# Performance work log

Hardware: AMD Instinct MI355X
Metric: run time of the kernel (lower is better)

## Reference

```python
import jax, jax.numpy as jnp
import numpy as np

GRID_SIZE = 8
MARGIN = 1.0
NUM_NEG = 8
SOS_NEG = 8
LOSS_LAMBDA = 1.0
D_INTER = 4  # d1_inter_num == d2_inter_num == 4 in the source
IMG = 512    # image side in pixels (H * grid_size)


def warp_points(pts, homo):
    ph = jnp.concatenate([pts, jnp.ones_like(pts[..., :1])], axis=-1)  # B,N,3
    q = jnp.einsum('bij,bnj->bni', homo, ph)
    return q[..., :2] / (q[..., 2:3] + 1e-8)


def inv_sim_vec(d1, d2):
    # 2 - 2*<d1,d2> == squared L2 distance for unit-norm descriptors
    return 2.0 - 2.0 * jnp.sum(d1 * d2, axis=-1)


def inv_sim_mat(d1, d2):
    return 2.0 - 2.0 * jnp.einsum('bnc,bmc->bnm', d1, d2)


def sq_dist_mat(p1, p2):
    # squared Euclidean distance; monotone in distance so topk indices and
    # radius comparisons (vs radius**2) match the original exactly.
    n1 = jnp.sum(p1 * p1, axis=-1)
    n2 = jnp.sum(p2 * p2, axis=-1)
    d = n1[:, :, None] + n2[:, None, :] - 2.0 * jnp.einsum('bnd,bmd->bnm', p1, p2)
    return jnp.maximum(d, 0.0)


def topk_smallest(x, k):
    v, i = jax.lax.top_k(-x, k)
    return -v, i


def create_coo_grid(h, w, grid_size):
    ys, xs = jnp.meshgrid(jnp.arange(h, dtype=jnp.float32), jnp.arange(w, dtype=jnp.float32), indexing='ij')
    return jnp.stack([(xs + 0.5) * grid_size, (ys + 0.5) * grid_size], axis=-1).reshape(-1, 2)  # HW,2 (x,y)


def sample_descriptors(desc, kp, grid_size):
    # desc: B,C,H,W; kp: B,N,2 (x,y) image coords. Bilinear sample + L2 normalize.
    b, c, h, w = desc.shape
    x = kp[..., 0] / grid_size - 0.5
    y = kp[..., 1] / grid_size - 0.5
    x0 = jnp.floor(x); y0 = jnp.floor(y)
    wx = x - x0; wy = y - y0
    x0i = jnp.clip(x0.astype(jnp.int32), 0, w - 1); x1i = jnp.clip(x0i + 1, 0, w - 1)
    y0i = jnp.clip(y0.astype(jnp.int32), 0, h - 1); y1i = jnp.clip(y0i + 1, 0, h - 1)
    dflat = desc.transpose(0, 2, 3, 1).reshape(b, h * w, c)  # B,HW,C
    bi = jnp.arange(b)[:, None]
    g = lambda yi, xi: dflat[bi, yi * w + xi]  # B,N,C
    out = ((1 - wx) * (1 - wy))[..., None] * g(y0i, x0i) \
        + (wx * (1 - wy))[..., None] * g(y0i, x1i) \
        + ((1 - wx) * wy)[..., None] * g(y1i, x0i) \
        + (wx * wy)[..., None] * g(y1i, x1i)
    return out / (jnp.linalg.norm(out, axis=-1, keepdims=True) + 1e-8)


def setup_inputs():
    key = jax.random.key(0)
    k1, k2, k3, k4 = jax.random.split(key, 4)
    b, n, c, h, w = 4, 1024, 128, 64, 64
    kp1 = jax.random.uniform(k1, (b, n, 2), dtype=jnp.float32) * (IMG - 1.0)
    kp1_desc = jax.random.normal(k2, (b, n, c), dtype=jnp.float32)
    kp1_desc = kp1_desc / jnp.linalg.norm(kp1_desc, axis=-1, keepdims=True)
    desc2 = jax.random.normal(k3, (b, c, h, w), dtype=jnp.float32)
    homo12 = jnp.broadcast_to(jnp.eye(3, dtype=jnp.float32), (b, 3, 3)) + 0.005 * jax.random.normal(k4, (b, 3, 3), dtype=jnp.float32)
    w_kp1 = jnp.clip(warp_points(kp1, homo12), 0.0, IMG - 1.0)
    return {'kp1': kp1, 'w_kp1': w_kp1, 'kp1_desc': kp1_desc, 'desc2': desc2, 'homo12': homo12}


def reference(kp1, w_kp1, kp1_desc, desc2, homo12):
    b, n, c = kp1_desc.shape
    _, _, h, w = desc2.shape
    hw = h * w
    gs = GRID_SIZE
    bi = jnp.arange(b)[:, None]

    w_kp1_desc = sample_descriptors(desc2, w_kp1, gs)                 # B,N,C
    positive_sim = inv_sim_vec(kp1_desc, w_kp1_desc)                  # B,N

    coo = jnp.broadcast_to(create_coo_grid(h, w, gs), (b, hw, 2))     # B,HW,2
    # 4 nearest grid cells of each kp1, warped into image 2
    _, kp1_cell_ids = topk_smallest(sq_dist_mat(kp1, coo), D_INTER)   # B,N,4
    kp1_cells = coo[bi, kp1_cell_ids.reshape(b, -1)]                  # B,4N,2
    w_kp1_cells = warp_points(kp1_cells, homo12)                      # B,4N,2
    _, kp2_cell_ids = topk_smallest(sq_dist_mat(w_kp1_cells, coo), D_INTER)  # B,4N,4
    mask = jnp.zeros((b, n * D_INTER, hw), dtype=jnp.float32)
    mask = mask.at[jnp.arange(b)[:, None, None], jnp.arange(n * D_INTER)[None, :, None], kp2_cell_ids].set(1.0)
    neigh_mask = mask.reshape(b, n, D_INTER, hw).sum(axis=2)          # B,N,HW

    desc2_flat = desc2.transpose(0, 2, 3, 1).reshape(b, hw, c)
    desc_sim = inv_sim_mat(kp1_desc, desc2_flat) + neigh_mask * 5.0   # B,N,HW
    neg_sim, _ = topk_smallest(desc_sim, NUM_NEG)                     # B,N,num_neg
    fos = jnp.mean(jnp.maximum(positive_sim[:, :, None] - neg_sim + MARGIN, 0.0) ** 2)

    radius2 = (gs * np.sqrt(2.0) + 0.1) ** 2
    kp1_sim = inv_sim_mat(kp1_desc, kp1_desc) + (sq_dist_mat(kp1, kp1) <= radius2).astype(jnp.float32) * 5.0
    w_kp1_sim = inv_sim_mat(w_kp1_desc, w_kp1_desc) + (sq_dist_mat(w_kp1, w_kp1) <= radius2).astype(jnp.float32) * 5.0
    _, kp1_neg_ids = topk_smallest(kp1_sim, SOS_NEG)                  # B,N,sos_neg
    _, w_kp1_neg_ids = topk_smallest(w_kp1_sim, SOS_NEG)
    b3 = jnp.arange(b)[:, None, None]
    kp1_neg_desc = kp1_desc[b3, kp1_neg_ids]                          # B,N,sos_neg,C
    w_kp1_neg_desc = w_kp1_desc[b3, w_kp1_neg_ids]
    sos = inv_sim_vec(kp1_desc[:, :, None, :], kp1_neg_desc) - inv_sim_vec(w_kp1_desc[:, :, None, :], w_kp1_neg_desc)
    sos = jnp.mean(jnp.sqrt(jnp.sum(sos ** 2, axis=-1)))
    return (fos + sos) * LOSS_LAMBDA
```

## Files before the change

kernel.cpp:

```cpp
#include <hip/hip_runtime.h>

#define NB 4
#define NN 1024
#define NCCH 128
#define NH 64
#define NW 64
#define NHW 4096

constexpr float RADIUS2 = 130.27274173013714f;

typedef __attribute__((ext_vector_type(8))) short short8v;
typedef __attribute__((ext_vector_type(4))) float f32x4;

__device__ __forceinline__ unsigned short f2bf(float f) {
    unsigned u = __float_as_uint(f);
    unsigned r = u + 0x7FFFu + ((u >> 16) & 1u);
    return (unsigned short)(r >> 16);
}
__device__ __forceinline__ float bf2f(unsigned short h) {
    return __uint_as_float(((unsigned)h) << 16);
}

__device__ __forceinline__ void bsort8(float* v) {
    #pragma unroll
    for (int d = 4; d >= 1; d >>= 1) {
        #pragma unroll
        for (int i = 0; i < 8; ++i) {
            if ((i & d) == 0) {
                float x = v[i], y = v[i + d];
                v[i] = fminf(x, y);
                v[i + d] = fmaxf(x, y);
            }
        }
    }
}
__device__ __forceinline__ void merge8(const float* a, const float* b, float* o) {
    #pragma unroll
    for (int k = 0; k < 8; ++k) o[k] = fminf(a[k], b[7 - k]);
    bsort8(o);
}

__device__ __forceinline__ void nearest4(float x, float y, int out_ids[4]) {
    float u = x * 0.125f - 0.5f;
    float v = y * 0.125f - 0.5f;
    u = fminf(fmaxf(u, -1e6f), 1e6f);
    v = fminf(fmaxf(v, -1e6f), 1e6f);
    int iu = (int)floorf(u);
    int iv = (int)floorf(v);
    int xlo = min(max(iu - 2, 0), 60);
    int xhi = max(min(iu + 3, 63), 3);
    int ylo = min(max(iv - 2, 0), 60);
    int yhi = max(min(iv + 3, 63), 3);
    float bd0 = 1e30f, bd1 = 1e30f, bd2 = 1e30f, bd3 = 1e30f;
    int bi0 = 0, bi1 = 0, bi2 = 0, bi3 = 0;
    for (int yy = ylo; yy <= yhi; ++yy) {
        float dy = y - ((float)yy + 0.5f) * 8.0f;
        float dy2 = dy * dy;
        for (int xx = xlo; xx <= xhi; ++xx) {
            float dx = x - ((float)xx + 0.5f) * 8.0f;
            float d = dx * dx + dy2;
            int id = (yy << 6) | xx;
            if (d < bd3) {
                if (d < bd2) {
                    bd3 = bd2; bi3 = bi2;
                    if (d < bd1) {
                        bd2 = bd1; bi2 = bi1;
                        if (d < bd0) { bd1 = bd0; bi1 = bi0; bd0 = d; bi0 = id; }
                        else         { bd1 = d;  bi1 = id; }
                    } else { bd2 = d; bi2 = id; }
                } else { bd3 = d; bi3 = id; }
            }
        }
    }
    out_ids[0] = bi0; out_ids[1] = bi1; out_ids[2] = bi2; out_ids[3] = bi3;
}

__global__ __launch_bounds__(256) void sample_kernel(
    const float* __restrict__ kp1, const float* __restrict__ w_kp1,
    const float* __restrict__ kp1_desc, const float* __restrict__ desc2,
    unsigned short* __restrict__ khi, unsigned short* __restrict__ klo,
    unsigned short* __restrict__ whi, unsigned short* __restrict__ wlo,
    float* __restrict__ pos_sim)
{
    int lane = threadIdx.x & 63;
    int wid = blockIdx.x * 4 + (threadIdx.x >> 6);
    if (wid >= NB * NN) return;
    int b = wid >> 10;

    float px = w_kp1[wid * 2 + 0], py = w_kp1[wid * 2 + 1];
    float fx = px * 0.125f - 0.5f, fy = py * 0.125f - 0.5f;
    float fx0 = floorf(fx), fy0 = floorf(fy);
    float wx = fx - fx0, wy = fy - fy0;
    int x0 = min(max((int)fx0, 0), NW - 1);
    int x1 = min(x0 + 1, NW - 1);
    int y0 = min(max((int)fy0, 0), NH - 1);
    int y1 = min(y0 + 1, NH - 1);
    float w00 = (1.f - wx) * (1.f - wy), w01 = wx * (1.f - wy);
    float w10 = (1.f - wx) * wy,         w11 = wx * wy;
    int i00 = y0 * NW + x0, i01 = y0 * NW + x1;
    int i10 = y1 * NW + x0, i11 = y1 * NW + x1;

    const float* d2 = desc2 + (size_t)b * NCCH * NHW;
    const float* p0 = d2 + (size_t)lane * NHW;
    const float* p1 = d2 + (size_t)(lane + 64) * NHW;
    float o0 = w00 * p0[i00] + w01 * p0[i01] + w10 * p0[i10] + w11 * p0[i11];
    float o1 = w00 * p1[i00] + w01 * p1[i01] + w10 * p1[i10] + w11 * p1[i11];
    float nrm = o0 * o0 + o1 * o1;
    #pragma unroll
    for (int off = 32; off > 0; off >>= 1) nrm += __shfl_xor(nrm, off, 64);
    float inv = 1.0f / (sqrtf(nrm) + 1e-8f);
    o0 *= inv; o1 *= inv;

    float a0 = kp1_desc[(size_t)wid * NCCH + lane];
    float a1 = kp1_desc[(size_t)wid * NCCH + lane + 64];
    float dot = a0 * o0 + a1 * o1;
    #pragma unroll
    for (int off = 32; off > 0; off >>= 1) dot += __shfl_xor(dot, off, 64);

    size_t base = (size_t)wid * NCCH;
    unsigned short h;
    h = f2bf(a0); khi[base + lane] = h;      klo[base + lane] = f2bf(a0 - bf2f(h));
    h = f2bf(a1); khi[base + lane + 64] = h; klo[base + lane + 64] = f2bf(a1 - bf2f(h));
    h = f2bf(o0); whi[base + lane] = h;      wlo[base + lane] = f2bf(o0 - bf2f(h));
    h = f2bf(o1); whi[base + lane + 64] = h; wlo[base + lane + 64] = f2bf(o1 - bf2f(h));
    if (lane == 0) pos_sim[wid] = 2.0f - 2.0f * dot;
}

__global__ __launch_bounds__(256) void d2split_kernel(
    const float* __restrict__ desc2,
    unsigned short* __restrict__ d2hi, unsigned short* __restrict__ d2lo)
{
    __shared__ float sT[64][130];
    int b = blockIdx.x >> 6;
    int hw0 = (blockIdx.x & 63) * 64;
    int t = threadIdx.x;
    int hwl = t & 63, cg = t >> 6;
    const float* src = desc2 + (size_t)b * NCCH * NHW + hw0 + hwl;
    #pragma unroll 4
    for (int i = 0; i < 32; ++i) {
        int c = cg * 32 + i;
        sT[hwl][c] = src[(size_t)c * NHW];
    }
    __syncthreads();
    int hw = t >> 2, cseg = (t & 3) * 32;
    unsigned short* dh = d2hi + ((size_t)b * NHW + hw0 + hw) * NCCH + cseg;
    unsigned short* dl = d2lo + ((size_t)b * NHW + hw0 + hw) * NCCH + cseg;
    #pragma unroll 4
    for (int i = 0; i < 32; ++i) {
        float f = sT[hw][cseg + i];
        unsigned short h = f2bf(f);
        dh[i] = h;
        dl[i] = f2bf(f - bf2f(h));
    }
}

__global__ __launch_bounds__(256) void mask_kernel(
    const float* __restrict__ kp1, const float* __restrict__ homo,
    int* __restrict__ mask_ids)
{
    int g = blockIdx.x * blockDim.x + threadIdx.x;
    if (g >= NB * NN) return;
    int b = g >> 10;
    float x = kp1[g * 2], y = kp1[g * 2 + 1];
    const float* H = homo + b * 9;
    int c4[4];
    nearest4(x, y, c4);
    int out[16];
    #pragma unroll
    for (int k = 0; k < 4; ++k) {
        int id = c4[k];
        float cx = ((float)(id & 63) + 0.5f) * 8.0f;
        float cy = ((float)(id >> 6) + 0.5f) * 8.0f;
        float q0 = H[0] * cx + H[1] * cy + H[2];
        float q1 = H[3] * cx + H[4] * cy + H[5];
        float q2 = H[6] * cx + H[7] * cy + H[8];
        float iz = 1.0f / (q2 + 1e-8f);
        nearest4(q0 * iz, q1 * iz, out + 4 * k);
    }
    #pragma unroll
    for (int k = 0; k < 16; ++k) mask_ids[(size_t)g * 16 + k] = out[k];
}

__global__ __launch_bounds__(256, 4) void simtop_fused(
    const unsigned short* __restrict__ khi, const unsigned short* __restrict__ klo,
    const unsigned short* __restrict__ whi, const unsigned short* __restrict__ wlo,
    const unsigned short* __restrict__ d2hi, const unsigned short* __restrict__ d2lo,
    const float* __restrict__ kp1, const float* __restrict__ w_kp1,
    const int* __restrict__ mask_ids,
    float* __restrict__ fosP, float* __restrict__ sosAP, float* __restrict__ sosBP)
{
    __shared__ float sChunk[16][257];
    __shared__ int   sMask[16][16];
    __shared__ float sCx[256], sCy[256];
    __shared__ float sRx[16], sRy[16];

    int tid = threadIdx.x;
    int bid = blockIdx.x;

    int mode, cs, rg, b, nchunk, colbase, outStride;
    const unsigned short *AH, *AL, *BH, *BL;
    const float* coords = nullptr;
    float* outP;
    if (bid < 1024) {
        mode = 0; cs = bid & 3; rg = (bid >> 2) & 63; b = bid >> 8;
        nchunk = 4; colbase = cs * 1024;
        AH = khi + (size_t)b * NN * NCCH;  AL = klo + (size_t)b * NN * NCCH;
        BH = d2hi + (size_t)b * NHW * NCCH; BL = d2lo + (size_t)b * NHW * NCCH;
        outP = fosP; outStride = 32;
    } else if (bid < 1536) {
        int id = bid - 1024;
        mode = 1; cs = id & 1; rg = (id >> 1) & 63; b = id >> 7;
        nchunk = 2; colbase = cs * 512;
        AH = khi + (size_t)b * NN * NCCH;  AL = klo + (size_t)b * NN * NCCH;
        BH = AH; BL = AL;
        coords = kp1; outP = sosAP; outStride = 16;
    } else {
        int id = bid - 1536;
        mode = 2; cs = id & 1; rg = (id >> 1) & 63; b = id >> 7;
        nchunk = 2; colbase = cs * 512;
        AH = whi + (size_t)b * NN * NCCH;  AL = wlo + (size_t)b * NN * NCCH;
        BH = AH; BL = AL;
        coords = w_kp1; outP = sosBP; outStride = 16;
    }
    int row0 = rg * 16;

    int lane = tid & 63, wg = tid >> 6;
    int lrow = lane & 15, lgrp = lane >> 4;
    int srow = tid & 15, sgrp = tid >> 4;

    short8v ahi[4], alo[4];
    {
        const unsigned short* aH = AH + (size_t)(row0 + lrow) * NCCH + lgrp * 8;
        const unsigned short* aL = AL + (size_t)(row0 + lrow) * NCCH + lgrp * 8;
        #pragma unroll
        for (int s = 0; s < 4; ++s) {
            ahi[s] = *(const short8v*)(aH + s * 32);
            alo[s] = *(const short8v*)(aL + s * 32);
        }
    }

    if (mode == 0) {
        sMask[tid >> 4][tid & 15] =
            mask_ids[((size_t)b * NN + row0 + (tid >> 4)) * 16 + (tid & 15)];
    } else if (tid < 16) {
        sRx[tid] = coords[((size_t)b * NN + row0 + tid) * 2];
        sRy[tid] = coords[((size_t)b * NN + row0 + tid) * 2 + 1];
    }

    float loc[8];
    #pragma unroll
    for (int k = 0; k < 8; ++k) loc[k] = 1e30f;

    for (int ch = 0; ch < nchunk; ++ch) {
        int cglob = colbase + ch * 256;
        __syncthreads();

        int colq = cglob + wg * 64;
        #pragma unroll
        for (int nt = 0; nt < 4; ++nt) {
            const unsigned short* bH = BH + (size_t)(colq + nt * 16 + lrow) * NCCH + lgrp * 8;
            const unsigned short* bL = BL + (size_t)(colq + nt * 16 + lrow) * NCCH + lgrp * 8;
            f32x4 acc = {0.f, 0.f, 0.f, 0.f};
            #pragma unroll
            for (int s = 0; s < 4; ++s) {
                short8v bhv = *(const short8v*)(bH + s * 32);
                short8v blv = *(const short8v*)(bL + s * 32);
                acc = __builtin_amdgcn_mfma_f32_16x16x32_bf16(ahi[s], bhv, acc, 0, 0, 0);
                acc = __builtin_amdgcn_mfma_f32_16x16x32_bf16(ahi[s], blv, acc, 0, 0, 0);
                acc = __builtin_amdgcn_mfma_f32_16x16x32_bf16(alo[s], bhv, acc, 0, 0, 0);
            }
            #pragma unroll
            for (int r = 0; r < 4; ++r)
                sChunk[lgrp * 4 + r][wg * 64 + nt * 16 + lrow] = 2.0f - 2.0f * acc[r];
        }
        __syncthreads();

        if (mode == 0) {
            int r = tid >> 4, k = tid & 15;
            int id = sMask[r][k] - cglob;
            if (id >= 0 && id < 256) atomicAdd(&sChunk[r][id], 5.0f);
        } else {
            sCx[tid] = coords[((size_t)b * NN + cglob + tid) * 2];
            sCy[tid] = coords[((size_t)b * NN + cglob + tid) * 2 + 1];
        }
        __syncthreads();

        float rx = 0.f, ry = 0.f;
        if (mode != 0) { rx = sRx[srow]; ry = sRy[srow]; }
        #pragma unroll
        for (int j = 0; j < 16; ++j) {
            int cl = sgrp * 16 + j;
            float v = sChunk[srow][cl];
            if (mode != 0) {
                float dx = rx - sCx[cl], dy = ry - sCy[cl];
                if (dx * dx + dy * dy <= RADIUS2) v += 5.0f;
            }
            if (v < loc[7]) {
                loc[7] = v;
                #pragma unroll
                for (int p = 7; p > 0; --p) {
                    if (loc[p - 1] > loc[p]) {
                        float t = loc[p - 1]; loc[p - 1] = loc[p]; loc[p] = t;
                    }
                }
            }
        }
    }

    __syncthreads();
    float* mg = &sChunk[0][0];
    #pragma unroll
    for (int k = 0; k < 8; ++k) mg[srow * 130 + sgrp * 8 + k] = loc[k];
    __syncthreads();
    #pragma unroll
    for (int step = 1; step < 16; step <<= 1) {
        if ((sgrp & (2 * step - 1)) == 0) {
            float a[8], bb[8], o[8];
            #pragma unroll
            for (int k = 0; k < 8; ++k) {
                a[k]  = mg[srow * 130 + sgrp * 8 + k];
                bb[k] = mg[srow * 130 + (sgrp + step) * 8 + k];
            }
            merge8(a, bb, o);
            #pragma unroll
            for (int k = 0; k < 8; ++k) mg[srow * 130 + sgrp * 8 + k] = o[k];
        }
        __syncthreads();
    }
    if (tid < 16) {
        size_t row = (size_t)b * NN + row0 + tid;
        #pragma unroll
        for (int k = 0; k < 8; ++k)
            outP[row * outStride + cs * 8 + k] = mg[tid * 130 + k];
    }
}

__global__ __launch_bounds__(256) void frow_kernel(
    const float* __restrict__ fosP, const float* __restrict__ sosAP,
    const float* __restrict__ sosBP, const float* __restrict__ pos_sim,
    float* __restrict__ frow, float* __restrict__ srow)
{
    int row = blockIdx.x * 256 + threadIdx.x;
    if (row >= NB * NN) return;

    float l0[8], l1[8], l2[8], l3[8], t0[8], t1[8], m[8];
    const float4* fp = (const float4*)(fosP + (size_t)row * 32);
    float4 q;
    q = fp[0]; l0[0]=q.x; l0[1]=q.y; l0[2]=q.z; l0[3]=q.w;
    q = fp[1]; l0[4]=q.x; l0[5]=q.y; l0[6]=q.z; l0[7]=q.w;
    q = fp[2]; l1[0]=q.x; l1[1]=q.y; l1[2]=q.z; l1[3]=q.w;
    q = fp[3]; l1[4]=q.x; l1[5]=q.y; l1[6]=q.z; l1[7]=q.w;
    q = fp[4]; l2[0]=q.x; l2[1]=q.y; l2[2]=q.z; l2[3]=q.w;
    q = fp[5]; l2[4]=q.x; l2[5]=q.y; l2[6]=q.z; l2[7]=q.w;
    q = fp[6]; l3[0]=q.x; l3[1]=q.y; l3[2]=q.z; l3[3]=q.w;
    q = fp[7]; l3[4]=q.x; l3[5]=q.y; l3[6]=q.z; l3[7]=q.w;
    merge8(l0, l1, t0); merge8(l2, l3, t1); merge8(t0, t1, m);

    float p = pos_sim[row], fs = 0.f;
    #pragma unroll
    for (int k = 0; k < 8; ++k) {
        float h = fmaxf(p - m[k] + 1.0f, 0.f);
        fs += h * h;
    }

    const float4* ap = (const float4*)(sosAP + (size_t)row * 16);
    q = ap[0]; l0[0]=q.x; l0[1]=q.y; l0[2]=q.z; l0[3]=q.w;
    q = ap[1]; l0[4]=q.x; l0[5]=q.y; l0[6]=q.z; l0[7]=q.w;
    q = ap[2]; l1[0]=q.x; l1[1]=q.y; l1[2]=q.z; l1[3]=q.w;
    q = ap[3]; l1[4]=q.x; l1[5]=q.y; l1[6]=q.z; l1[7]=q.w;
    merge8(l0, l1, t0);
    const float4* bp = (const float4*)(sosBP + (size_t)row * 16);
    q = bp[0]; l2[0]=q.x; l2[1]=q.y; l2[2]=q.z; l2[3]=q.w;
    q = bp[1]; l2[4]=q.x; l2[5]=q.y; l2[6]=q.z; l2[7]=q.w;
    q = bp[2]; l3[0]=q.x; l3[1]=q.y; l3[2]=q.z; l3[3]=q.w;
    q = bp[3]; l3[4]=q.x; l3[5]=q.y; l3[6]=q.z; l3[7]=q.w;
    merge8(l2, l3, t1);

    float acc = 0.f;
    #pragma unroll
    for (int k = 0; k < 8; ++k) {
        float d = t0[k] - t1[k];
        acc += d * d;
    }
    frow[row] = fs;
    srow[row] = sqrtf(acc);
}

__global__ __launch_bounds__(256) void freduce_kernel(
    const float* __restrict__ frow, const float* __restrict__ srow,
    float* __restrict__ outp)
{
    __shared__ float sf[256], ss[256];
    int t = threadIdx.x;
    float f = 0.f, s = 0.f;
    for (int i = t; i < NB * NN; i += 256) { f += frow[i]; s += srow[i]; }
    sf[t] = f; ss[t] = s;
    __syncthreads();
    for (int o = 128; o > 0; o >>= 1) {
        if (t < o) { sf[t] += sf[t + o]; ss[t] += ss[t + o]; }
        __syncthreads();
    }
    if (t == 0)
        outp[0] = sf[0] / (float)(NB * NN * 8) + ss[0] / (float)(NB * NN);
}

extern "C" void kernel_launch(void* const* d_in, const int* in_sizes, int n_in,
                              void* d_out, int out_size, void* d_ws, size_t ws_size,
                              hipStream_t stream) {
    const float* kp1      = (const float*)d_in[0];
    const float* w_kp1    = (const float*)d_in[1];
    const float* kp1_desc = (const float*)d_in[2];
    const float* desc2    = (const float*)d_in[3];
    const float* homo     = (const float*)d_in[4];
    float* outp = (float*)d_out;

    char* ws = (char*)d_ws;
    size_t o = 0;
    unsigned short* khi  = (unsigned short*)(ws + o); o += (size_t)NB * NN * NCCH * 2;
    unsigned short* klo  = (unsigned short*)(ws + o); o += (size_t)NB * NN * NCCH * 2;
    unsigned short* whi  = (unsigned short*)(ws + o); o += (size_t)NB * NN * NCCH * 2;
    unsigned short* wlo  = (unsigned short*)(ws + o); o += (size_t)NB * NN * NCCH * 2;
    unsigned short* d2hi = (unsigned short*)(ws + o); o += (size_t)NB * NHW * NCCH * 2;
    unsigned short* d2lo = (unsigned short*)(ws + o); o += (size_t)NB * NHW * NCCH * 2;
    float* pos_sim = (float*)(ws + o); o += (size_t)NB * NN * 4;
    float* fosP    = (float*)(ws + o); o += (size_t)NB * NN * 32 * 4;
    float* sosAP   = (float*)(ws + o); o += (size_t)NB * NN * 16 * 4;
    float* sosBP   = (float*)(ws + o); o += (size_t)NB * NN * 16 * 4;
    float* frow    = (float*)(ws + o); o += (size_t)NB * NN * 4;
    float* srow    = (float*)(ws + o); o += (size_t)NB * NN * 4;
    int*   mask_id = (int*)(ws + o);   o += (size_t)NB * NN * 16 * 4;

    sample_kernel<<<NB * NN / 4, 256, 0, stream>>>(kp1, w_kp1, kp1_desc, desc2,
                                                   khi, klo, whi, wlo, pos_sim);
    d2split_kernel<<<NB * 64, 256, 0, stream>>>(desc2, d2hi, d2lo);
    mask_kernel<<<NB * NN / 256, 256, 0, stream>>>(kp1, homo, mask_id);
    simtop_fused<<<2048, 256, 0, stream>>>(khi, klo, whi, wlo, d2hi, d2lo,
                                           kp1, w_kp1, mask_id,
                                           fosP, sosAP, sosBP);
    frow_kernel<<<16, 256, 0, stream>>>(fosP, sosAP, sosBP, pos_sim, frow, srow);
    freduce_kernel<<<1, 256, 0, stream>>>(frow, srow, outp);
}
```

Measured before the change: 211.8 us.

## Widen simtop row tiles to 32, fuse sample+mask, transpose desc2 for sampling

The similarity/top-k kernel now processes 32 rows per block using a 2x2 MFMA register tile, so each loaded B fragment is reused across two row tiles. This halves the grid and the B-operand global traffic. The d2split kernel is re-tiled with vectorized stores and optionally writes an fp32 HWC transpose of desc2, which the sampling path reads with coalesced row accesses instead of strided channel gathers. Sampling and mask computation are merged into one launch. The changes raise register and shared memory pressure in the top-k kernel and add an extra fp32 write of desc2, which may be skipped if the workspace is too small.

```diff
diff --git a/kernel.cpp b/kernel.cpp
--- a/kernel.cpp
+++ b/kernel.cpp
@@ -75,16 +75,88 @@
     out_ids[0] = bi0; out_ids[1] = bi1; out_ids[2] = bi2; out_ids[3] = bi3;
 }
 
-__global__ __launch_bounds__(256) void sample_kernel(
+__global__ __launch_bounds__(256) void d2split_kernel(
+    const float* __restrict__ desc2,
+    unsigned short* __restrict__ d2hi, unsigned short* __restrict__ d2lo,
+    float* __restrict__ d2T, int use_t)
+{
+    __shared__ float sT[64][33];
+    int bid = blockIdx.x;
+    int b = bid >> 8;
+    int rem = bid & 255;
+    int hw0 = (rem >> 2) * 64;
+    int c0 = (rem & 3) * 32;
+    int t = threadIdx.x;
+
+    {
+        int lane = t & 63, cg = t >> 6;
+        const float* src = desc2 + (size_t)b * NCCH * NHW + hw0 + lane;
+        #pragma unroll
+        for (int i = 0; i < 8; ++i) {
+            int cl = cg * 8 + i;
+            sT[lane][cl] = src[(size_t)(c0 + cl) * NHW];
+        }
+    }
+    __syncthreads();
+    {
+        int hw = t >> 2, q = t & 3;
+        size_t base = ((size_t)b * NHW + hw0 + hw) * NCCH + c0 + q * 8;
+        unsigned short hb[8], lb[8];
+        float fb[8];
+        #pragma unroll
+        for (int i = 0; i < 8; ++i) {
+            float f = sT[hw][q * 8 + i];
+            unsigned short h = f2bf(f);
+            hb[i] = h;
+            lb[i] = f2bf(f - bf2f(h));
+            fb[i] = f;
+        }
+        *(short8v*)(d2hi + base) = *(short8v*)hb;
+        *(short8v*)(d2lo + base) = *(short8v*)lb;
+        if (use_t) {
+            *(float4*)(d2T + base) = *(float4*)&fb[0];
+            *(float4*)(d2T + base + 4) = *(float4*)&fb[4];
+        }
+    }
+}
+
+__global__ __launch_bounds__(256) void sample_mask_kernel(
     const float* __restrict__ kp1, const float* __restrict__ w_kp1,
     const float* __restrict__ kp1_desc, const float* __restrict__ desc2,
+    const float* __restrict__ d2T, int use_t,
+    const float* __restrict__ homo,
     unsigned short* __restrict__ khi, unsigned short* __restrict__ klo,
     unsigned short* __restrict__ whi, unsigned short* __restrict__ wlo,
-    float* __restrict__ pos_sim)
+    float* __restrict__ pos_sim, int* __restrict__ mask_ids)
 {
+    int bid = blockIdx.x;
+    if (bid >= 1024) {
+        int g = (bid - 1024) * 256 + threadIdx.x;
+        if (g >= NB * NN) return;
+        int b = g >> 10;
+        float x = kp1[g * 2], y = kp1[g * 2 + 1];
+        const float* H = homo + b * 9;
+        int c4[4];
+        nearest4(x, y, c4);
+        int out[16];
+        #pragma unroll
+        for (int k = 0; k < 4; ++k) {
+            int id = c4[k];
+            float cx = ((float)(id & 63) + 0.5f) * 8.0f;
+            float cy = ((float)(id >> 6) + 0.5f) * 8.0f;
+            float q0 = H[0] * cx + H[1] * cy + H[2];
+            float q1 = H[3] * cx + H[4] * cy + H[5];
+            float q2 = H[6] * cx + H[7] * cy + H[8];
+            float iz = 1.0f / (q2 + 1e-8f);
+            nearest4(q0 * iz, q1 * iz, out + 4 * k);
+        }
+        #pragma unroll
+        for (int k = 0; k < 16; ++k) mask_ids[(size_t)g * 16 + k] = out[k];
+        return;
+    }
+
     int lane = threadIdx.x & 63;
-    int wid = blockIdx.x * 4 + (threadIdx.x >> 6);
-    if (wid >= NB * NN) return;
+    int wid = bid * 4 + (threadIdx.x >> 6);
     int b = wid >> 10;
 
     float px = w_kp1[wid * 2 + 0], py = w_kp1[wid * 2 + 1];
@@ -100,11 +172,23 @@
     int i00 = y0 * NW + x0, i01 = y0 * NW + x1;
     int i10 = y1 * NW + x0, i11 = y1 * NW + x1;
 
-    const float* d2 = desc2 + (size_t)b * NCCH * NHW;
-    const float* p0 = d2 + (size_t)lane * NHW;
-    const float* p1 = d2 + (size_t)(lane + 64) * NHW;
-    float o0 = w00 * p0[i00] + w01 * p0[i01] + w10 * p0[i10] + w11 * p0[i11];
-    float o1 = w00 * p1[i00] + w01 * p1[i01] + w10 * p1[i10] + w11 * p1[i11];
+    float o0, o1;
+    if (use_t) {
+        const float* base = d2T + (size_t)b * NHW * NCCH;
+        const float* r00 = base + (size_t)i00 * NCCH;
+        const float* r01 = base + (size_t)i01 * NCCH;
+        const float* r10 = base + (size_t)i10 * NCCH;
+        const float* r11 = base + (size_t)i11 * NCCH;
+        o0 = w00 * r00[lane] + w01 * r01[lane] + w10 * r10[lane] + w11 * r11[lane];
+        o1 = w00 * r00[lane + 64] + w01 * r01[lane + 64]
+           + w10 * r10[lane + 64] + w11 * r11[lane + 64];
+    } else {
+        const float* d2 = desc2 + (size_t)b * NCCH * NHW;
+        const float* p0 = d2 + (size_t)lane * NHW;
+        const float* p1 = d2 + (size_t)(lane + 64) * NHW;
+        o0 = w00 * p0[i00] + w01 * p0[i01] + w10 * p0[i10] + w11 * p0[i11];
+        o1 = w00 * p1[i00] + w01 * p1[i01] + w10 * p1[i10] + w11 * p1[i11];
+    }
     float nrm = o0 * o0 + o1 * o1;
     #pragma unroll
     for (int off = 32; off > 0; off >>= 1) nrm += __shfl_xor(nrm, off, 64);
@@ -124,61 +208,6 @@
     h = f2bf(o0); whi[base + lane] = h;      wlo[base + lane] = f2bf(o0 - bf2f(h));
     h = f2bf(o1); whi[base + lane + 64] = h; wlo[base + lane + 64] = f2bf(o1 - bf2f(h));
     if (lane == 0) pos_sim[wid] = 2.0f - 2.0f * dot;
-}
-
-__global__ __launch_bounds__(256) void d2split_kernel(
-    const float* __restrict__ desc2,
-    unsigned short* __restrict__ d2hi, unsigned short* __restrict__ d2lo)
-{
-    __shared__ float sT[64][130];
-    int b = blockIdx.x >> 6;
-    int hw0 = (blockIdx.x & 63) * 64;
-    int t = threadIdx.x;
-    int hwl = t & 63, cg = t >> 6;
-    const float* src = desc2 + (size_t)b * NCCH * NHW + hw0 + hwl;
-    #pragma unroll 4
-    for (int i = 0; i < 32; ++i) {
-        int c = cg * 32 + i;
-        sT[hwl][c] = src[(size_t)c * NHW];
-    }
-    __syncthreads();
-    int hw = t >> 2, cseg = (t & 3) * 32;
-    unsigned short* dh = d2hi + ((size_t)b * NHW + hw0 + hw) * NCCH + cseg;
-    unsigned short* dl = d2lo + ((size_t)b * NHW + hw0 + hw) * NCCH + cseg;
-    #pragma unroll 4
-    for (int i = 0; i < 32; ++i) {
-        float f = sT[hw][cseg + i];
-        unsigned short h = f2bf(f);
-        dh[i] = h;
-        dl[i] = f2bf(f - bf2f(h));
-    }
-}
-
-__global__ __launch_bounds__(256) void mask_kernel(
-    const float* __restrict__ kp1, const float* __restrict__ homo,
-    int* __restrict__ mask_ids)
-{
-    int g = blockIdx.x * blockDim.x + threadIdx.x;
-    if (g >= NB * NN) return;
-    int b = g >> 10;
-    float x = kp1[g * 2], y = kp1[g * 2 + 1];
-    const float* H = homo + b * 9;
-    int c4[4];
-    nearest4(x, y, c4);
-    int out[16];
-    #pragma unroll
-    for (int k = 0; k < 4; ++k) {
-        int id = c4[k];
-        float cx = ((float)(id & 63) + 0.5f) * 8.0f;
-        float cy = ((float)(id >> 6) + 0.5f) * 8.0f;
-        float q0 = H[0] * cx + H[1] * cy + H[2];
-        float q1 = H[3] * cx + H[4] * cy + H[5];
-        float q2 = H[6] * cx + H[7] * cy + H[8];
-        float iz = 1.0f / (q2 + 1e-8f);
-        nearest4(q0 * iz, q1 * iz, out + 4 * k);
-    }
-    #pragma unroll
-    for (int k = 0; k < 16; ++k) mask_ids[(size_t)g * 16 + k] = out[k];
 }
 
 __global__ __launch_bounds__(256, 4) void simtop_fused(
@@ -189,10 +218,10 @@
     const int* __restrict__ mask_ids,
     float* __restrict__ fosP, float* __restrict__ sosAP, float* __restrict__ sosBP)
 {
-    __shared__ float sChunk[16][257];
-    __shared__ int   sMask[16][16];
+    __shared__ float sChunk[32][257];
+    __shared__ int   sMask[32][16];
     __shared__ float sCx[256], sCy[256];
-    __shared__ float sRx[16], sRy[16];
+    __shared__ float sRx[32], sRy[32];
 
     int tid = threadIdx.x;
     int bid = blockIdx.x;
@@ -201,48 +230,53 @@
     const unsigned short *AH, *AL, *BH, *BL;
     const float* coords = nullptr;
     float* outP;
-    if (bid < 1024) {
-        mode = 0; cs = bid & 3; rg = (bid >> 2) & 63; b = bid >> 8;
+    if (bid < 512) {
+        mode = 0; b = bid >> 7; int rem = bid & 127;
+        cs = rem & 3; rg = rem >> 2;
         nchunk = 4; colbase = cs * 1024;
         AH = khi + (size_t)b * NN * NCCH;  AL = klo + (size_t)b * NN * NCCH;
         BH = d2hi + (size_t)b * NHW * NCCH; BL = d2lo + (size_t)b * NHW * NCCH;
         outP = fosP; outStride = 32;
-    } else if (bid < 1536) {
-        int id = bid - 1024;
-        mode = 1; cs = id & 1; rg = (id >> 1) & 63; b = id >> 7;
+    } else if (bid < 768) {
+        int id = bid - 512;
+        mode = 1; b = id >> 6; int rem = id & 63;
+        cs = rem & 1; rg = rem >> 1;
         nchunk = 2; colbase = cs * 512;
         AH = khi + (size_t)b * NN * NCCH;  AL = klo + (size_t)b * NN * NCCH;
         BH = AH; BL = AL;
         coords = kp1; outP = sosAP; outStride = 16;
     } else {
-        int id = bid - 1536;
-        mode = 2; cs = id & 1; rg = (id >> 1) & 63; b = id >> 7;
+        int id = bid - 768;
+        mode = 2; b = id >> 6; int rem = id & 63;
+        cs = rem & 1; rg = rem >> 1;
         nchunk = 2; colbase = cs * 512;
         AH = whi + (size_t)b * NN * NCCH;  AL = wlo + (size_t)b * NN * NCCH;
         BH = AH; BL = AL;
         coords = w_kp1; outP = sosBP; outStride = 16;
     }
-    int row0 = rg * 16;
+    int row0 = rg * 32;
 
     int lane = tid & 63, wg = tid >> 6;
     int lrow = lane & 15, lgrp = lane >> 4;
-    int srow = tid & 15, sgrp = tid >> 4;
-
-    short8v ahi[4], alo[4];
-    {
-        const unsigned short* aH = AH + (size_t)(row0 + lrow) * NCCH + lgrp * 8;
-        const unsigned short* aL = AL + (size_t)(row0 + lrow) * NCCH + lgrp * 8;
+    int srow = tid & 31, sgrp = tid >> 5;
+
+    short8v ahi[2][4], alo[2][4];
+    #pragma unroll
+    for (int rt = 0; rt < 2; ++rt) {
+        const unsigned short* aH = AH + (size_t)(row0 + rt * 16 + lrow) * NCCH + lgrp * 8;
+        const unsigned short* aL = AL + (size_t)(row0 + rt * 16 + lrow) * NCCH + lgrp * 8;
         #pragma unroll
         for (int s = 0; s < 4; ++s) {
-            ahi[s] = *(const short8v*)(aH + s * 32);
-            alo[s] = *(const short8v*)(aL + s * 32);
+            ahi[rt][s] = *(const short8v*)(aH + s * 32);
+            alo[rt][s] = *(const short8v*)(aL + s * 32);
         }
     }
 
     if (mode == 0) {
-        sMask[tid >> 4][tid & 15] =
-            mask_ids[((size_t)b * NN + row0 + (tid >> 4)) * 16 + (tid & 15)];
-    } else if (tid < 16) {
+        for (int e = tid; e < 512; e += 256)
+            sMask[e >> 4][e & 15] =
+                mask_ids[((size_t)b * NN + row0 + (e >> 4)) * 16 + (e & 15)];
+    } else if (tid < 32) {
         sRx[tid] = coords[((size_t)b * NN + row0 + tid) * 2];
         sRy[tid] = coords[((size_t)b * NN + row0 + tid) * 2 + 1];
     }
@@ -257,28 +291,48 @@
 
         int colq = cglob + wg * 64;
         #pragma unroll
-        for (int nt = 0; nt < 4; ++nt) {
-            const unsigned short* bH = BH + (size_t)(colq + nt * 16 + lrow) * NCCH + lgrp * 8;
-            const unsigned short* bL = BL + (size_t)(colq + nt * 16 + lrow) * NCCH + lgrp * 8;
-            f32x4 acc = {0.f, 0.f, 0.f, 0.f};
+        for (int np = 0; np < 2; ++np) {
+            const unsigned short* b0H = BH + (size_t)(colq + (np * 2 + 0) * 16 + lrow) * NCCH + lgrp * 8;
+            const unsigned short* b0L = BL + (size_t)(colq + (np * 2 + 0) * 16 + lrow) * NCCH + lgrp * 8;
+            const unsigned short* b1H = BH + (size_t)(colq + (np * 2 + 1) * 16 + lrow) * NCCH + lgrp * 8;
+            const unsigned short* b1L = BL + (size_t)(colq + (np * 2 + 1) * 16 + lrow) * NCCH + lgrp * 8;
+            f32x4 a00 = {0.f, 0.f, 0.f, 0.f}, a01 = {0.f, 0.f, 0.f, 0.f};
+            f32x4 a10 = {0.f, 0.f, 0.f, 0.f}, a11 = {0.f, 0.f, 0.f, 0.f};
             #pragma unroll
             for (int s = 0; s < 4; ++s) {
-                short8v bhv = *(const short8v*)(bH + s * 32);
-                short8v blv = *(const short8v*)(bL + s * 32);
-                acc = __builtin_amdgcn_mfma_f32_16x16x32_bf16(ahi[s], bhv, acc, 0, 0, 0);
-                acc = __builtin_amdgcn_mfma_f32_16x16x32_bf16(ahi[s], blv, acc, 0, 0, 0);
-                acc = __builtin_amdgcn_mfma_f32_16x16x32_bf16(alo[s], bhv, acc, 0, 0, 0);
+                short8v bh0 = *(const short8v*)(b0H + s * 32);
+                short8v bl0 = *(const short8v*)(b0L + s * 32);
+                short8v bh1 = *(const short8v*)(b1H + s * 32);
+                short8v bl1 = *(const short8v*)(b1L + s * 32);
+                a00 = __builtin_amdgcn_mfma_f32_16x16x32_bf16(ahi[0][s], bh0, a00, 0, 0, 0);
+                a10 = __builtin_amdgcn_mfma_f32_16x16x32_bf16(ahi[1][s], bh0, a10, 0, 0, 0);
+                a01 = __builtin_amdgcn_mfma_f32_16x16x32_bf16(ahi[0][s], bh1, a01, 0, 0, 0);
+                a11 = __builtin_amdgcn_mfma_f32_16x16x32_bf16(ahi[1][s], bh1, a11, 0, 0, 0);
+                a00 = __builtin_amdgcn_mfma_f32_16x16x32_bf16(ahi[0][s], bl0, a00, 0, 0, 0);
+                a10 = __builtin_amdgcn_mfma_f32_16x16x32_bf16(ahi[1][s], bl0, a10, 0, 0, 0);
+                a01 = __builtin_amdgcn_mfma_f32_16x16x32_bf16(ahi[0][s], bl1, a01, 0, 0, 0);
+                a11 = __builtin_amdgcn_mfma_f32_16x16x32_bf16(ahi[1][s], bl1, a11, 0, 0, 0);
+                a00 = __builtin_amdgcn_mfma_f32_16x16x32_bf16(alo[0][s], bh0, a00, 0, 0, 0);
+                a10 = __builtin_amdgcn_mfma_f32_16x16x32_bf16(alo[1][s], bh0, a10, 0, 0, 0);
+                a01 = __builtin_amdgcn_mfma_f32_16x16x32_bf16(alo[0][s], bh1, a01, 0, 0, 0);
+                a11 = __builtin_amdgcn_mfma_f32_16x16x32_bf16(alo[1][s], bh1, a11, 0, 0, 0);
             }
             #pragma unroll
-            for (int r = 0; r < 4; ++r)
-                sChunk[lgrp * 4 + r][wg * 64 + nt * 16 + lrow] = 2.0f - 2.0f * acc[r];
+            for (int r = 0; r < 4; ++r) {
+                sChunk[lgrp * 4 + r][wg * 64 + (np * 2 + 0) * 16 + lrow]      = 2.0f - 2.0f * a00[r];
+                sChunk[16 + lgrp * 4 + r][wg * 64 + (np * 2 + 0) * 16 + lrow] = 2.0f - 2.0f * a10[r];
+                sChunk[lgrp * 4 + r][wg * 64 + (np * 2 + 1) * 16 + lrow]      = 2.0f - 2.0f * a01[r];
+                sChunk[16 + lgrp * 4 + r][wg * 64 + (np * 2 + 1) * 16 + lrow] = 2.0f - 2.0f * a11[r];
+            }
         }
         __syncthreads();
 
         if (mode == 0) {
-            int r = tid >> 4, k = tid & 15;
-            int id = sMask[r][k] - cglob;
-            if (id >= 0 && id < 256) atomicAdd(&sChunk[r][id], 5.0f);
+            for (int e = tid; e < 512; e += 256) {
+                int r = e >> 4;
+                int id = sMask[r][e & 15] - cglob;
+                if (id >= 0 && id < 256) atomicAdd(&sChunk[r][id], 5.0f);
+            }
         } else {
             sCx[tid] = coords[((size_t)b * NN + cglob + tid) * 2];
             sCy[tid] = coords[((size_t)b * NN + cglob + tid) * 2 + 1];
@@ -288,8 +342,8 @@
         float rx = 0.f, ry = 0.f;
         if (mode != 0) { rx = sRx[srow]; ry = sRy[srow]; }
         #pragma unroll
-        for (int j = 0; j < 16; ++j) {
-            int cl = sgrp * 16 + j;
+        for (int j = 0; j < 32; ++j) {
+            int cl = sgrp * 32 + j;
             float v = sChunk[srow][cl];
             if (mode != 0) {
                 float dx = rx - sCx[cl], dy = ry - sCy[cl];
@@ -310,28 +364,28 @@
     __syncthreads();
     float* mg = &sChunk[0][0];
     #pragma unroll
-    for (int k = 0; k < 8; ++k) mg[srow * 130 + sgrp * 8 + k] = loc[k];
+    for (int k = 0; k < 8; ++k) mg[srow * 67 + sgrp * 8 + k] = loc[k];
     __syncthreads();
     #pragma unroll
-    for (int step = 1; step < 16; step <<= 1) {
+    for (int step = 1; step < 8; step <<= 1) {
         if ((sgrp & (2 * step - 1)) == 0) {
             float a[8], bb[8], o[8];
             #pragma unroll
             for (int k = 0; k < 8; ++k) {
-                a[k]  = mg[srow * 130 + sgrp * 8 + k];
-                bb[k] = mg[srow * 130 + (sgrp + step) * 8 + k];
+                a[k]  = mg[srow * 67 + sgrp * 8 + k];
+                bb[k] = mg[srow * 67 + (sgrp + step) * 8 + k];
             }
             merge8(a, bb, o);
             #pragma unroll
-            for (int k = 0; k < 8; ++k) mg[srow * 130 + sgrp * 8 + k] = o[k];
+            for (int k = 0; k < 8; ++k) mg[srow * 67 + sgrp * 8 + k] = o[k];
         }
         __syncthreads();
     }
-    if (tid < 16) {
+    if (tid < 32) {
         size_t row = (size_t)b * NN + row0 + tid;
         #pragma unroll
         for (int k = 0; k < 8; ++k)
-            outP[row * outStride + cs * 8 + k] = mg[tid * 130 + k];
+            outP[row * outStride + cs * 8 + k] = mg[tid * 67 + k];
     }
 }
 
@@ -429,12 +483,17 @@
     float* frow    = (float*)(ws + o); o += (size_t)NB * NN * 4;
     float* srow    = (float*)(ws + o); o += (size_t)NB * NN * 4;
     int*   mask_id = (int*)(ws + o);   o += (size_t)NB * NN * 16 * 4;
-
-    sample_kernel<<<NB * NN / 4, 256, 0, stream>>>(kp1, w_kp1, kp1_desc, desc2,
-                                                   khi, klo, whi, wlo, pos_sim);
-    d2split_kernel<<<NB * 64, 256, 0, stream>>>(desc2, d2hi, d2lo);
-    mask_kernel<<<NB * NN / 256, 256, 0, stream>>>(kp1, homo, mask_id);
-    simtop_fused<<<2048, 256, 0, stream>>>(khi, klo, whi, wlo, d2hi, d2lo,
+    float* d2T     = (float*)(ws + o);
+    size_t need_t  = o + (size_t)NB * NHW * NCCH * 4;
+    int use_t = (ws_size >= need_t) ? 1 : 0;
+    if (!use_t) d2T = (float*)ws;
+
+    d2split_kernel<<<NB * 256, 256, 0, stream>>>(desc2, d2hi, d2lo, d2T, use_t);
+    sample_mask_kernel<<<1040, 256, 0, stream>>>(kp1, w_kp1, kp1_desc, desc2,
+                                                 d2T, use_t, homo,
+                                                 khi, klo, whi, wlo,
+                                                 pos_sim, mask_id);
+    simtop_fused<<<1024, 256, 0, stream>>>(khi, klo, whi, wlo, d2hi, d2lo,
                                            kp1, w_kp1, mask_id,
                                            fosP, sosAP, sosBP);
     frow_kernel<<<16, 256, 0, stream>>>(fosP, sosAP, sosBP, pos_sim, frow, srow);
```

Result: faster. 199.7 us (-5.7%).
